# Optimization experiments

Measured on AMD Instinct MI355X. Metric: run time of the kernel, lower is better.

## Reference

```python
import jax, jax.numpy as jnp
import numpy as np

E = 1024
H = 16
F = 4096
B, S = 4, 2048
LN_EPS = 1e-5


def setup_inputs() -> dict:
    key = jax.random.key(0)
    ks = jax.random.split(key, 12)
    sE = 1.0 / np.sqrt(E)
    sF = 1.0 / np.sqrt(F)
    return {
        "x": jax.random.normal(ks[0], (B, S, E), dtype=jnp.float32),
        # attention projections (torch Linear weight layout [out,in], bias=False)
        "Wq": jax.random.uniform(ks[1], (E, E), jnp.float32, -sE, sE),
        "Wk": jax.random.uniform(ks[2], (E, E), jnp.float32, -sE, sE),
        "Wv": jax.random.uniform(ks[3], (E, E), jnp.float32, -sE, sE),
        "Wo": jax.random.uniform(ks[4], (E, E), jnp.float32, -sE, sE),
        # LayerNorms
        "g1": jnp.ones((E,), jnp.float32),
        "b1": jnp.zeros((E,), jnp.float32),
        "g2": jnp.ones((E,), jnp.float32),
        "b2": jnp.zeros((E,), jnp.float32),
        # FFN (classical): linear1 [F,E], linear2 [E,F]
        "W1": jax.random.uniform(ks[5], (F, E), jnp.float32, -sE, sE),
        "bb1": jax.random.uniform(ks[6], (F,), jnp.float32, -sE, sE),
        "W2": jax.random.uniform(ks[7], (E, F), jnp.float32, -sF, sF),
        "bb2": jax.random.uniform(ks[8], (F,), jnp.float32, -sF, sF)[:E] * 0 + jax.random.uniform(ks[9], (E,), jnp.float32, -sF, sF),
    }


def _layernorm(x, g, b):
    mu = jnp.mean(x, axis=-1, keepdims=True)
    var = jnp.mean(jnp.square(x - mu), axis=-1, keepdims=True)
    return (x - mu) * jax.lax.rsqrt(var + LN_EPS) * g + b


def reference(x, Wq, Wk, Wv, Wo, g1, b1, g2, b2, W1, bb1, W2, bb2):
    b, s, _ = x.shape
    hd = E // H
    # projections: torch Linear is x @ W.T
    q = (x @ Wq.T).reshape(b, s, H, hd).transpose(0, 2, 1, 3)  # [B,H,S,hd]
    k = (x @ Wk.T).reshape(b, s, H, hd).transpose(0, 2, 1, 3)
    v = (x @ Wv.T).reshape(b, s, H, hd).transpose(0, 2, 1, 3)
    scores = jnp.einsum('bhqd,bhkd->bhqk', q, k) / jnp.sqrt(jnp.float32(hd))
    probs = jax.nn.softmax(scores, axis=-1)
    attn = jnp.einsum('bhqk,bhkd->bhqd', probs, v)
    attn = attn.transpose(0, 2, 1, 3).reshape(b, s, E)
    attn_out = attn @ Wo.T
    # residual + LN (dropout=0 / eval)
    h = _layernorm(x + attn_out, g1, b1)
    # FFN
    ffn = jax.nn.relu(h @ W1.T + bb1) @ W2.T + bb2
    return _layernorm(h + ffn, g2, b2)
```

## Files before the change

kernel.cpp:

```cpp
#include <hip/hip_runtime.h>
#include <stdint.h>

#define E_DIM   1024
#define H_NUM   16
#define HD      64
#define F_DIM   4096
#define B_NUM   4
#define S_LEN   2048
#define M_ROWS  (B_NUM * S_LEN)
#define QKV_LD  3072

typedef unsigned short u16;
typedef __bf16 bf16_t;
typedef bf16_t  bf16x8 __attribute__((ext_vector_type(8)));
typedef u16     u16x8  __attribute__((ext_vector_type(8)));
typedef float   f32x4  __attribute__((ext_vector_type(4)));
typedef float   f32x16 __attribute__((ext_vector_type(16)));
typedef unsigned u32x4 __attribute__((ext_vector_type(4)));

#define AS1 __attribute__((address_space(1)))
#define AS3 __attribute__((address_space(3)))

__device__ __forceinline__ void gload_lds16(const void* g, void* l) {
    __builtin_amdgcn_global_load_lds((AS1 void*)g, (AS3 void*)l, 16, 0, 0);
}

__device__ __forceinline__ u16 f2b(float f) {
    union { float f; unsigned u; } a; a.f = f;
    unsigned u = a.u + 0x7fffu + ((a.u >> 16) & 1u);
    return (u16)(u >> 16);
}
__device__ __forceinline__ float b2f(u16 v) {
    union { unsigned u; float f; } a; a.u = ((unsigned)v) << 16;
    return a.f;
}

__device__ __forceinline__ unsigned cvt_pk_bf16(float lo, float hi) {
    unsigned r;
    asm("v_cvt_pk_bf16_f32 %0, %1, %2" : "=v"(r) : "v"(lo), "v"(hi));
    return r;
}

__device__ __forceinline__ int swz_c(int row) {
    return ((row & 7) << 4) ^ ((row & 8) << 2);
}
__device__ __forceinline__ int swz8(int row) {
    return (row & 7) << 4;
}

#define VM_WAIT(n) asm volatile("s_waitcnt vmcnt(" #n ")" ::: "memory")
#define SC_LOG2E 0.1803368801111204f

struct CastArgs {
    const float* src[7];
    u16* dst[7];
    float scale[7];
    unsigned cum4[8];
};

__global__ __launch_bounds__(256) void cast_multi(CastArgs a) {
    const int total = a.cum4[7];
    const int stride = gridDim.x * blockDim.x;
    for (int i = blockIdx.x * blockDim.x + threadIdx.x; i < total; i += stride) {
        int s = 0;
#pragma unroll
        for (int k = 1; k < 7; ++k) s += (i >= (int)a.cum4[k]);
        const int off = i - (int)a.cum4[s];
        const float sc = a.scale[s];
        float4 v = reinterpret_cast<const float4*>(a.src[s])[off];
        ushort4 o;
        o.x = f2b(v.x * sc); o.y = f2b(v.y * sc); o.z = f2b(v.z * sc); o.w = f2b(v.w * sc);
        reinterpret_cast<ushort4*>(a.dst[s])[off] = o;
    }
}

__device__ __forceinline__ void store_c(float* C, size_t idx, float v) { C[idx] = v; }
__device__ __forceinline__ void store_c(u16* C, size_t idx, float v)   { C[idx] = f2b(v); }

template <typename OutT, bool RELU, bool HASBIAS, int K, bool VSPLIT>
__global__ __launch_bounds__(512, 4)
void gemm2(const u16* __restrict__ A, const u16* __restrict__ B,
           OutT* __restrict__ C, const float* __restrict__ bias,
           char* __restrict__ VtG, int M, int N) {
    constexpr int NT = K / 32;
    __shared__ __align__(16) char smem[3 * 24576];

    const int tid  = threadIdx.x;
    const int lane = tid & 63, wave = tid >> 6;
    const int lr   = lane & 15, kh = lane >> 4;
    const int wr   = wave >> 2, wc = wave & 3;

    const int nwg = gridDim.x * gridDim.y;
    int wg = blockIdx.y * gridDim.x + blockIdx.x;
    const int cpx = nwg >> 3;
    wg = (wg & 7) * cpx + (wg >> 3);
    const int bx = wg % gridDim.x, by = wg / gridDim.x;
    const int row0 = by * 128, col0 = bx * 256;

    const int srow = tid >> 2, scolb = (tid & 3) * 16;
    const char* Ag  = (const char*)(A + (size_t)(row0 + srow) * K) + scolb;
    const char* Bg0 = (const char*)(B + (size_t)(col0 + srow) * K) + scolb;
    const char* Bg1 = (const char*)(B + (size_t)(col0 + 128 + srow) * K) + scolb;
    const int ldsw = wave * 1024;

    auto stage = [&](int t) {
        char* s = smem + (t % 3) * 24576;
        const size_t ko = (size_t)t * 64;
        gload_lds16(Ag + ko,  s + ldsw);
        gload_lds16(Bg0 + ko, s + 8192 + ldsw);
        gload_lds16(Bg1 + ko, s + 16384 + ldsw);
    };

    f32x4 acc[4][4] = {};
    stage(0); stage(1);

    for (int t = 0; t < NT; ++t) {
        if (t + 1 < NT) VM_WAIT(3);
        else            VM_WAIT(0);
        __builtin_amdgcn_s_barrier();
        __builtin_amdgcn_sched_barrier(0);
        if (t + 2 < NT) stage(t + 2);

        const char* s = smem + (t % 3) * 24576;
        bf16x8 af[4], bf[4];
#pragma unroll
        for (int m = 0; m < 4; ++m)
            af[m] = *(const bf16x8*)(s + (wr * 64 + m * 16 + lr) * 64 + kh * 16);
#pragma unroll
        for (int n = 0; n < 4; ++n)
            bf[n] = *(const bf16x8*)(s + 8192 + (wc * 64 + n * 16 + lr) * 64 + kh * 16);

        __builtin_amdgcn_s_setprio(1);
#pragma unroll
        for (int m = 0; m < 4; ++m)
#pragma unroll
            for (int n = 0; n < 4; ++n)
                acc[m][n] = __builtin_amdgcn_mfma_f32_16x16x32_bf16(af[m], bf[n], acc[m][n], 0, 0, 0);
        __builtin_amdgcn_s_setprio(0);
    }

    if (VSPLIT && col0 >= 2048) {
#pragma unroll
        for (int m = 0; m < 4; ++m) {
#pragma unroll
            for (int n = 0; n < 4; ++n) {
                const int colv = col0 - 2048 + wc * 64 + n * 16 + lr;
                const int h = colv >> 6, d = colv & 63;
                const int rowq = row0 + wr * 64 + m * 16 + kh * 4;
                const int bq = rowq >> 11, sq = rowq & 2047;
                const int kvt = sq >> 6, kl = sq & 63;
                const int g = kl >> 4, qb = kl & 12;
                const int slotq = ((qb & 4) << 1) | ((qb & 8) >> 1) | (qb & 3);
                const size_t byte_off = ((size_t)((bq * H_NUM + h) * HD + d) << 12)
                                        + kvt * 128 + ((((g << 4) + slotq) << 1) ^ swz8(d));
                const u16 p0 = f2b(acc[m][n][0]), p1 = f2b(acc[m][n][1]);
                const u16 p2 = f2b(acc[m][n][2]), p3 = f2b(acc[m][n][3]);
                uint2 pk;
                pk.x = (unsigned)p0 | ((unsigned)p1 << 16);
                pk.y = (unsigned)p2 | ((unsigned)p3 << 16);
                *(uint2*)(VtG + byte_off) = pk;
            }
        }
        return;
    }

#pragma unroll
    for (int m = 0; m < 4; ++m) {
#pragma unroll
        for (int n = 0; n < 4; ++n) {
            int col = col0 + wc * 64 + n * 16 + lr;
            float bv = 0.f;
            if constexpr (HASBIAS) bv = bias[col];
#pragma unroll
            for (int r = 0; r < 4; ++r) {
                int row = row0 + wr * 64 + m * 16 + kh * 4 + r;
                float v = acc[m][n][r] + bv;
                if constexpr (RELU) v = fmaxf(v, 0.f);
                store_c(C, (size_t)row * N + col, v);
            }
        }
    }
}

template <typename OutT, bool RELU, bool HASBIAS, int K>
__global__ __launch_bounds__(256, 3)
void gemm2h(const u16* __restrict__ A, const u16* __restrict__ B,
            OutT* __restrict__ C, const float* __restrict__ bias,
            int M, int N) {
    constexpr int NT = K / 32;
    __shared__ __align__(16) char smem[3 * 16384];

    const int tid  = threadIdx.x;
    const int lane = tid & 63, wave = tid >> 6;
    const int lr   = lane & 15, kh = lane >> 4;
    const int wr   = wave >> 1, wc = wave & 1;

    const int nwg = gridDim.x * gridDim.y;
    int wg = blockIdx.y * gridDim.x + blockIdx.x;
    const int cpx = nwg >> 3;
    wg = (wg & 7) * cpx + (wg >> 3);
    const int bx = wg % gridDim.x, by = wg / gridDim.x;
    const int row0 = by * 128, col0 = bx * 128;

    const int srow = tid >> 2;
    const int scolb = (tid & 3) * 16;
    const char* Ag = (const char*)(A + (size_t)(row0 + srow) * K) + scolb;
    const char* Bg = (const char*)(B + (size_t)(col0 + srow) * K) + scolb;
    const size_t rstep = (size_t)64 * K * 2;

    auto do_stage = [&](int t) {
        char* s = smem + (t % 3) * 16384;
        const size_t ko = (size_t)t * 64;
        gload_lds16(Ag + ko,         s + tid * 16);
        gload_lds16(Ag + rstep + ko, s + 4096 + tid * 16);
        gload_lds16(Bg + ko,         s + 8192 + tid * 16);
        gload_lds16(Bg + rstep + ko, s + 12288 + tid * 16);
    };

    f32x4 acc[4][4] = {};
    do_stage(0); do_stage(1);

    for (int t = 0; t < NT; ++t) {
        if (t + 1 < NT) VM_WAIT(4);
        else            VM_WAIT(0);
        __builtin_amdgcn_s_barrier();
        __builtin_amdgcn_sched_barrier(0);
        if (t + 2 < NT) do_stage(t + 2);

        const char* s = smem + (t % 3) * 16384;
        bf16x8 af[4], bf[4];
#pragma unroll
        for (int m = 0; m < 4; ++m)
            af[m] = *(const bf16x8*)(s + (wr * 64 + m * 16 + lr) * 64 + kh * 16);
#pragma unroll
        for (int n = 0; n < 4; ++n)
            bf[n] = *(const bf16x8*)(s + 8192 + (wc * 64 + n * 16 + lr) * 64 + kh * 16);

        __builtin_amdgcn_s_setprio(1);
#pragma unroll
        for (int m = 0; m < 4; ++m)
#pragma unroll
            for (int n = 0; n < 4; ++n)
                acc[m][n] = __builtin_amdgcn_mfma_f32_16x16x32_bf16(af[m], bf[n], acc[m][n], 0, 0, 0);
        __builtin_amdgcn_s_setprio(0);
    }

#pragma unroll
    for (int m = 0; m < 4; ++m) {
#pragma unroll
        for (int n = 0; n < 4; ++n) {
            int col = col0 + wc * 64 + n * 16 + lr;
            float bv = 0.f;
            if constexpr (HASBIAS) bv = bias[col];
#pragma unroll
            for (int r = 0; r < 4; ++r) {
                int row = row0 + wr * 64 + m * 16 + kh * 4 + r;
                float v = acc[m][n][r] + bv;
                if constexpr (RELU) v = fmaxf(v, 0.f);
                store_c(C, (size_t)row * N + col, v);
            }
        }
    }
}

__global__ __launch_bounds__(256, 4)
void attn_kernel(const u16* __restrict__ QKV, const char* __restrict__ VtG,
                 u16* __restrict__ Ob) {
    __shared__ char Ks[2][64 * 128];
    __shared__ char Vt[2][64 * 128];

    const int tid  = threadIdx.x;
    const int lane = tid & 63, wave = tid >> 6;
    const int l31  = lane & 31, hi = lane >> 5;
    const int q0   = blockIdx.x * 128;
    const int h    = blockIdx.y;
    const int b    = blockIdx.z;

    const u16* Q  = QKV;
    const u16* Kp = QKV + 1024;

    const size_t qrow = (size_t)(b * S_LEN + q0 + wave * 32 + l31);
    bf16x8 qf[4];
#pragma unroll
    for (int c = 0; c < 4; ++c)
        qf[c] = *(const bf16x8*)(Q + qrow * QKV_LD + h * HD + c * 16 + hi * 8);

    f32x16 o0 = {}, o1 = {};
    float l_run = 0.f;

    const char* Kg  = (const char*)(Kp + (size_t)(b * S_LEN) * QKV_LD + h * HD);
    const char* Vgb = VtG + ((size_t)((b * H_NUM + h) * HD) << 12);

    int st_row[2], st_colb[2], st_lds[2], kst_colb[2];
#pragma unroll
    for (int j = 0; j < 2; ++j) {
        const int ob = (wave * 2 + j) * 1024 + lane * 16;
        st_row[j]   = ob >> 7;
        st_colb[j]  = ob & 127;
        kst_colb[j] = (ob & 127) ^ swz_c(st_row[j]);
        st_lds[j]   = (wave * 2 + j) * 1024;
    }
    const int krd = l31 * 128;
    const int vrd = l31 * 128;

#pragma unroll
    for (int j = 0; j < 2; ++j) {
        gload_lds16(Kg + (size_t)st_row[j] * (QKV_LD * 2) + kst_colb[j], Ks[0] + st_lds[j]);
        gload_lds16(Vgb + (size_t)st_row[j] * 4096 + st_colb[j],         Vt[0] + st_lds[j]);
    }
    __syncthreads();

    const int NT = S_LEN / 64;
    for (int t = 0; t < NT; ++t) {
        const int cur = t & 1;
        if (t < NT - 1) {
            const int kv0n = (t + 1) * 64;
#pragma unroll
            for (int j = 0; j < 2; ++j) {
                gload_lds16(Kg + (size_t)(kv0n + st_row[j]) * (QKV_LD * 2) + kst_colb[j],
                            Ks[cur ^ 1] + st_lds[j]);
                gload_lds16(Vgb + (size_t)st_row[j] * 4096 + (t + 1) * 128 + st_colb[j],
                            Vt[cur ^ 1] + st_lds[j]);
            }
        }

#pragma unroll
        for (int half = 0; half < 2; ++half) {
            const char* ksb = Ks[cur] + half * 4096 + krd;
            f32x16 st = {};
#pragma unroll
            for (int c = 0; c < 4; ++c) {
                bf16x8 kf = *(const bf16x8*)(ksb + ((c * 32 + hi * 16) ^ swz_c(l31)));
                st = __builtin_amdgcn_mfma_f32_32x32x16_bf16(kf, qf[c], st, 0, 0, 0);
            }

            float rs0 = 0.f, rs1 = 0.f, rs2 = 0.f, rs3 = 0.f;
#pragma unroll
            for (int i = 0; i < 16; i += 4) {
                st[i]     = exp2f(st[i]);
                st[i + 1] = exp2f(st[i + 1]);
                st[i + 2] = exp2f(st[i + 2]);
                st[i + 3] = exp2f(st[i + 3]);
                rs0 += st[i]; rs1 += st[i + 1]; rs2 += st[i + 2]; rs3 += st[i + 3];
            }
            float rs = (rs0 + rs1) + (rs2 + rs3);
            rs += __shfl_xor(rs, 32);
            l_run += rs;

            unsigned w[8];
#pragma unroll
            for (int i = 0; i < 8; ++i) w[i] = cvt_pk_bf16(st[2 * i], st[2 * i + 1]);

#pragma unroll
            for (int cc = 0; cc < 2; ++cc) {
                u32x4 fw;
                fw[0] = w[4 * cc];     fw[1] = w[4 * cc + 1];
                fw[2] = w[4 * cc + 2]; fw[3] = w[4 * cc + 3];
                bf16x8 pf = __builtin_bit_cast(bf16x8, fw);
                const int colb = (half * 64 + cc * 32 + hi * 16) ^ swz8(l31);
                bf16x8 v0 = *(const bf16x8*)(Vt[cur] + vrd + colb);
                bf16x8 v1 = *(const bf16x8*)(Vt[cur] + 4096 + vrd + colb);
                o0 = __builtin_amdgcn_mfma_f32_32x32x16_bf16(v0, pf, o0, 0, 0, 0);
                o1 = __builtin_amdgcn_mfma_f32_32x32x16_bf16(v1, pf, o1, 0, 0, 0);
            }
        }
        __syncthreads();
    }

    const float inv = 1.0f / l_run;
    unsigned m0[16], xx[16];
#pragma unroll
    for (int g = 0; g < 4; ++g)
#pragma unroll
        for (int u = 0; u < 2; ++u) {
            int r = g * 4 + 2 * u;
            m0[2 * g + u]     = cvt_pk_bf16(o0[r] * inv, o0[r + 1] * inv);
            m0[8 + 2 * g + u] = cvt_pk_bf16(o1[r] * inv, o1[r + 1] * inv);
        }
#pragma unroll
    for (int i = 0; i < 16; ++i) xx[i] = __shfl_xor(m0[i], 32);

    {
        unsigned full[8], sec[8];
#pragma unroll
        for (int g = 0; g < 4; ++g) {
            full[2 * g + 0] = hi ? xx[8 + 2 * g]     : m0[2 * g];
            full[2 * g + 1] = hi ? xx[8 + 2 * g + 1] : m0[2 * g + 1];
            sec[2 * g + 0]  = hi ? m0[8 + 2 * g]     : xx[2 * g];
            sec[2 * g + 1]  = hi ? m0[8 + 2 * g + 1] : xx[2 * g + 1];
        }
        u32x4 out0, out1, out2, out3;
        out0[0] = full[0]; out0[1] = full[1]; out0[2] = sec[0]; out0[3] = sec[1];
        out1[0] = full[2]; out1[1] = full[3]; out1[2] = sec[2]; out1[3] = sec[3];
        out2[0] = full[4]; out2[1] = full[5]; out2[2] = sec[4]; out2[3] = sec[5];
        out3[0] = full[6]; out3[1] = full[7]; out3[2] = sec[6]; out3[3] = sec[7];
        u16* op = Ob + qrow * E_DIM + h * HD + hi * 32;
        *(u32x4*)(op)      = out0;
        *(u32x4*)(op + 8)  = out1;
        *(u32x4*)(op + 16) = out2;
        *(u32x4*)(op + 24) = out3;
    }
}

template <typename XA, typename XB>
__device__ __forceinline__ float4 ld4(const XA* p, size_t idx) {
    if constexpr (sizeof(XA) == 2) {
        ushort4 v = reinterpret_cast<const ushort4*>(p)[idx];
        float4 o; o.x = b2f(v.x); o.y = b2f(v.y); o.z = b2f(v.z); o.w = b2f(v.w);
        return o;
    } else {
        return reinterpret_cast<const float4*>(p)[idx];
    }
}

template <typename XA, typename XB>
__global__ __launch_bounds__(256)
void add_ln(const XA* __restrict__ xa, const XB* __restrict__ xb2,
            const float* __restrict__ g, const float* __restrict__ be,
            float* __restrict__ of, u16* __restrict__ ob) {
    const int row = blockIdx.x;
    const int t = threadIdx.x;
    const int lane = t & 63, wave = t >> 6;

    float4 va = ld4<XA, XB>(xa + (size_t)row * E_DIM, t);
    float4 vb = ld4<XB, XA>(xb2 + (size_t)row * E_DIM, t);
    float v0 = va.x + vb.x, v1 = va.y + vb.y, v2 = va.z + vb.z, v3 = va.w + vb.w;
    float s  = v0 + v1 + v2 + v3;
    float s2 = v0 * v0 + v1 * v1 + v2 * v2 + v3 * v3;
#pragma unroll
    for (int m = 32; m >= 1; m >>= 1) {
        s  += __shfl_xor(s, m);
        s2 += __shfl_xor(s2, m);
    }
    __shared__ float red[8];
    if (lane == 0) { red[wave] = s; red[4 + wave] = s2; }
    __syncthreads();
    s  = red[0] + red[1] + red[2] + red[3];
    s2 = red[4] + red[5] + red[6] + red[7];

    float mu   = s * (1.0f / E_DIM);
    float var  = s2 * (1.0f / E_DIM) - mu * mu;
    float rstd = rsqrtf(var + 1e-5f);

    float4 gg = reinterpret_cast<const float4*>(g)[t];
    float4 bb = reinterpret_cast<const float4*>(be)[t];
    float y0 = (v0 - mu) * rstd * gg.x + bb.x;
    float y1 = (v1 - mu) * rstd * gg.y + bb.y;
    float y2 = (v2 - mu) * rstd * gg.z + bb.z;
    float y3 = (v3 - mu) * rstd * gg.w + bb.w;
    if (of) {
        float4 o; o.x = y0; o.y = y1; o.z = y2; o.w = y3;
        reinterpret_cast<float4*>(of + (size_t)row * E_DIM)[t] = o;
    }
    if (ob) {
        ushort4 o;
        o.x = f2b(y0); o.y = f2b(y1); o.z = f2b(y2); o.w = f2b(y3);
        reinterpret_cast<ushort4*>(ob + (size_t)row * E_DIM)[t] = o;
    }
}

extern "C" void kernel_launch(void* const* d_in, const int* in_sizes, int n_in,
                              void* d_out, int out_size, void* d_ws, size_t ws_size,
                              hipStream_t stream) {
    const float* x   = (const float*)d_in[0];
    const float* Wq  = (const float*)d_in[1];
    const float* Wk  = (const float*)d_in[2];
    const float* Wv  = (const float*)d_in[3];
    const float* Wo  = (const float*)d_in[4];
    const float* g1  = (const float*)d_in[5];
    const float* b1  = (const float*)d_in[6];
    const float* g2  = (const float*)d_in[7];
    const float* b2  = (const float*)d_in[8];
    const float* W1  = (const float*)d_in[9];
    const float* bb1 = (const float*)d_in[10];
    const float* W2  = (const float*)d_in[11];
    const float* bb2 = (const float*)d_in[12];
    float* out = (float*)d_out;

    char* ws = (char*)d_ws;
    const size_t MB = 1024ull * 1024ull;
    u16* wqkvb = (u16*)(ws + 0 * MB);
    u16* wob   = (u16*)(ws + 6 * MB);
    u16* w1b   = (u16*)(ws + 8 * MB);
    u16* w2b   = (u16*)(ws + 16 * MB);
    u16* xb    = (u16*)(ws + 24 * MB);
    u16* qkvb  = (u16*)(ws + 40 * MB);
    u16* attnb = (u16*)(ws + 88 * MB);
    u16* attno = (u16*)(ws + 104 * MB);
    u16* hb    = (u16*)(ws + 136 * MB);
    char* VtG  = (ws + 152 * MB);
    u16* ffn1  = (u16*)(ws + 24 * MB);
    u16* y2b   = (u16*)(ws + 104 * MB);

    dim3 blk(256);

    CastArgs ca;
    ca.src[0] = x;   ca.dst[0] = xb;                            ca.scale[0] = 1.f;
    ca.src[1] = Wq;  ca.dst[1] = wqkvb;                         ca.scale[1] = SC_LOG2E;
    ca.src[2] = Wk;  ca.dst[2] = wqkvb + E_DIM * E_DIM;         ca.scale[2] = 1.f;
    ca.src[3] = Wv;  ca.dst[3] = wqkvb + 2 * E_DIM * E_DIM;     ca.scale[3] = 1.f;
    ca.src[4] = Wo;  ca.dst[4] = wob;                           ca.scale[4] = 1.f;
    ca.src[5] = W1;  ca.dst[5] = w1b;                           ca.scale[5] = 1.f;
    ca.src[6] = W2;  ca.dst[6] = w2b;                           ca.scale[6] = 1.f;
    unsigned n4[7] = {M_ROWS * E_DIM / 4, E_DIM * E_DIM / 4, E_DIM * E_DIM / 4,
                      E_DIM * E_DIM / 4, E_DIM * E_DIM / 4, F_DIM * E_DIM / 4,
                      E_DIM * F_DIM / 4};
    ca.cum4[0] = 0;
    for (int i = 0; i < 7; ++i) ca.cum4[i + 1] = ca.cum4[i] + n4[i];
    cast_multi<<<dim3(2048), blk, 0, stream>>>(ca);

    dim3 blk5(512);
    gemm2<u16, false, false, E_DIM, true><<<dim3(QKV_LD / 256, M_ROWS / 128), blk5, 0, stream>>>(
        xb, wqkvb, qkvb, nullptr, VtG, M_ROWS, QKV_LD);

    attn_kernel<<<dim3(S_LEN / 128, H_NUM, B_NUM), blk, 0, stream>>>(qkvb, VtG, attnb);

    gemm2h<u16, false, false, E_DIM><<<dim3(E_DIM / 128, M_ROWS / 128), blk, 0, stream>>>(
        attnb, wob, attno, nullptr, M_ROWS, E_DIM);

    add_ln<float, u16><<<dim3(M_ROWS), blk, 0, stream>>>(x, attno, g1, b1, nullptr, hb);

    gemm2<u16, true, true, E_DIM, false><<<dim3(F_DIM / 256, M_ROWS / 128), blk5, 0, stream>>>(
        hb, w1b, ffn1, bb1, nullptr, M_ROWS, F_DIM);

    gemm2h<u16, false, true, F_DIM><<<dim3(E_DIM / 128, M_ROWS / 128), blk, 0, stream>>>(
        ffn1, w2b, y2b, bb2, M_ROWS, E_DIM);

    add_ln<u16, u16><<<dim3(M_ROWS), blk, 0, stream>>>(hb, y2b, g2, b2, out, nullptr);
}
```

Measured before the change: 383.6 us.

## Use 256x256-tile GEMM for FFN1 and read bf16 residual in first LayerNorm

Adds a gemm2w kernel with 512 threads computing a 256x256 output tile (8 waves, each 128x64) with triple-buffered LDS staging, and uses it for the FFN1 GEMM in place of the 128-row-tile gemm2. The larger tile raises arithmetic intensity and cuts global/L2 traffic for the biggest GEMM, in exchange for one workgroup per CU, 96KB of LDS and fewer workgroups (512). Separately, the first add+LayerNorm now reads the bf16 copy of x rather than fp32, halving that read at a small precision cost in the residual.

```diff
diff --git a/kernel.cpp b/kernel.cpp
--- a/kernel.cpp
+++ b/kernel.cpp
@@ -183,6 +183,86 @@
 }
 
 template <typename OutT, bool RELU, bool HASBIAS, int K>
+__global__ __launch_bounds__(512, 1)
+void gemm2w(const u16* __restrict__ A, const u16* __restrict__ B,
+            OutT* __restrict__ C, const float* __restrict__ bias,
+            int M, int N) {
+    constexpr int NT = K / 32;
+    __shared__ __align__(16) char smem[3 * 32768];
+
+    const int tid  = threadIdx.x;
+    const int lane = tid & 63, wave = tid >> 6;
+    const int lr   = lane & 15, kh = lane >> 4;
+    const int wr   = wave >> 2, wc = wave & 3;
+
+    const int nwg = gridDim.x * gridDim.y;
+    int wg = blockIdx.y * gridDim.x + blockIdx.x;
+    const int cpx = nwg >> 3;
+    wg = (wg & 7) * cpx + (wg >> 3);
+    const int bx = wg % gridDim.x, by = wg / gridDim.x;
+    const int row0 = by * 256, col0 = bx * 256;
+
+    const int srow = tid >> 2, scolb = (tid & 3) * 16;
+    const char* Ag = (const char*)(A + (size_t)(row0 + srow) * K) + scolb;
+    const char* Bg = (const char*)(B + (size_t)(col0 + srow) * K) + scolb;
+    const size_t rstep = (size_t)128 * K * 2;
+
+    auto stage = [&](int t) {
+        char* s = smem + (t % 3) * 32768;
+        const size_t ko = (size_t)t * 64;
+        gload_lds16(Ag + ko,          s + tid * 16);
+        gload_lds16(Ag + rstep + ko,  s + 8192 + tid * 16);
+        gload_lds16(Bg + ko,          s + 16384 + tid * 16);
+        gload_lds16(Bg + rstep + ko,  s + 24576 + tid * 16);
+    };
+
+    f32x4 acc[8][4] = {};
+    stage(0); stage(1);
+
+    for (int t = 0; t < NT; ++t) {
+        if (t + 1 < NT) VM_WAIT(4);
+        else            VM_WAIT(0);
+        __builtin_amdgcn_s_barrier();
+        __builtin_amdgcn_sched_barrier(0);
+        if (t + 2 < NT) stage(t + 2);
+
+        const char* s = smem + (t % 3) * 32768;
+        bf16x8 af[8], bf[4];
+#pragma unroll
+        for (int m = 0; m < 8; ++m)
+            af[m] = *(const bf16x8*)(s + (wr * 128 + m * 16 + lr) * 64 + kh * 16);
+#pragma unroll
+        for (int n = 0; n < 4; ++n)
+            bf[n] = *(const bf16x8*)(s + 16384 + (wc * 64 + n * 16 + lr) * 64 + kh * 16);
+
+        __builtin_amdgcn_s_setprio(1);
+#pragma unroll
+        for (int m = 0; m < 8; ++m)
+#pragma unroll
+            for (int n = 0; n < 4; ++n)
+                acc[m][n] = __builtin_amdgcn_mfma_f32_16x16x32_bf16(af[m], bf[n], acc[m][n], 0, 0, 0);
+        __builtin_amdgcn_s_setprio(0);
+    }
+
+#pragma unroll
+    for (int m = 0; m < 8; ++m) {
+#pragma unroll
+        for (int n = 0; n < 4; ++n) {
+            int col = col0 + wc * 64 + n * 16 + lr;
+            float bv = 0.f;
+            if constexpr (HASBIAS) bv = bias[col];
+#pragma unroll
+            for (int r = 0; r < 4; ++r) {
+                int row = row0 + wr * 128 + m * 16 + kh * 4 + r;
+                float v = acc[m][n][r] + bv;
+                if constexpr (RELU) v = fmaxf(v, 0.f);
+                store_c(C, (size_t)row * N + col, v);
+            }
+        }
+    }
+}
+
+template <typename OutT, bool RELU, bool HASBIAS, int K>
 __global__ __launch_bounds__(256, 3)
 void gemm2h(const u16* __restrict__ A, const u16* __restrict__ B,
             OutT* __restrict__ C, const float* __restrict__ bias,
@@ -402,7 +482,7 @@
     }
 }
 
-template <typename XA, typename XB>
+template <typename XA>
 __device__ __forceinline__ float4 ld4(const XA* p, size_t idx) {
     if constexpr (sizeof(XA) == 2) {
         ushort4 v = reinterpret_cast<const ushort4*>(p)[idx];
@@ -422,8 +502,8 @@
     const int t = threadIdx.x;
     const int lane = t & 63, wave = t >> 6;
 
-    float4 va = ld4<XA, XB>(xa + (size_t)row * E_DIM, t);
-    float4 vb = ld4<XB, XA>(xb2 + (size_t)row * E_DIM, t);
+    float4 va = ld4<XA>(xa + (size_t)row * E_DIM, t);
+    float4 vb = ld4<XB>(xb2 + (size_t)row * E_DIM, t);
     float v0 = va.x + vb.x, v1 = va.y + vb.y, v2 = va.z + vb.z, v3 = va.w + vb.w;
     float s  = v0 + v1 + v2 + v3;
     float s2 = v0 * v0 + v1 * v1 + v2 * v2 + v3 * v3;
@@ -518,10 +598,10 @@
     gemm2h<u16, false, false, E_DIM><<<dim3(E_DIM / 128, M_ROWS / 128), blk, 0, stream>>>(
         attnb, wob, attno, nullptr, M_ROWS, E_DIM);
 
-    add_ln<float, u16><<<dim3(M_ROWS), blk, 0, stream>>>(x, attno, g1, b1, nullptr, hb);
-
-    gemm2<u16, true, true, E_DIM, false><<<dim3(F_DIM / 256, M_ROWS / 128), blk5, 0, stream>>>(
-        hb, w1b, ffn1, bb1, nullptr, M_ROWS, F_DIM);
+    add_ln<u16, u16><<<dim3(M_ROWS), blk, 0, stream>>>(xb, attno, g1, b1, nullptr, hb);
+
+    gemm2w<u16, true, true, E_DIM><<<dim3(F_DIM / 256, M_ROWS / 256), blk5, 0, stream>>>(
+        hb, w1b, ffn1, bb1, M_ROWS, F_DIM);
 
     gemm2h<u16, false, true, F_DIM><<<dim3(E_DIM / 128, M_ROWS / 128), blk, 0, stream>>>(
         ffn1, w2b, y2b, bb2, M_ROWS, E_DIM);
```

After: 380.2 us. About the same (-0.9%).
